# Performance work log

Hardware: AMD Instinct MI355X
Metric: run time of the kernel (lower is better)

## Reference

```python
import jax, jax.numpy as jnp
import numpy as np

B, L, E, H, RR, BIO, NT, V, R = 16, 128, 256, 256, 128, 64, 3, 30000, 25


def setup_inputs() -> dict:
    key = jax.random.key(0)
    ks = jax.random.split(key, 24)
    s = 0.05
    n = jax.random.normal
    inp = {
        'tokens': jax.random.randint(ks[0], (B, L), 0, V),
        'bio_gold': jax.random.randint(ks[1], (B, L), 0, NT),
        'selection_gold': jax.random.uniform(ks[2], (B, L, R, L), jnp.float32),
        'word_emb': n(ks[3], (V, E), jnp.float32) * s,
        'W_ih_f': n(ks[4], (4 * H, E), jnp.float32) * s,
        'W_hh_f': n(ks[5], (4 * H, H), jnp.float32) * s,
        'b_f': n(ks[6], (4 * H,), jnp.float32) * s,
        'W_ih_b': n(ks[7], (4 * H, E), jnp.float32) * s,
        'W_hh_b': n(ks[8], (4 * H, H), jnp.float32) * s,
        'b_b': n(ks[9], (4 * H,), jnp.float32) * s,
        'emi_W': n(ks[10], (NT, H), jnp.float32) * s,
        'emi_b': n(ks[11], (NT,), jnp.float32) * s,
        'bio_emb': n(ks[12], (NT + 1, BIO), jnp.float32) * s,
        'sel_u_W': n(ks[13], (RR, H + BIO), jnp.float32) * s,
        'sel_u_b': n(ks[14], (RR,), jnp.float32) * s,
        'sel_v_W': n(ks[15], (RR, H + BIO), jnp.float32) * s,
        'sel_v_b': n(ks[16], (RR,), jnp.float32) * s,
        'sel_uv_W': n(ks[17], (RR, 2 * RR), jnp.float32) * s,
        'sel_uv_b': n(ks[18], (RR,), jnp.float32) * s,
        'rel_emb': n(ks[19], (R, RR), jnp.float32) * s,
        'crf_start': n(ks[20], (NT,), jnp.float32) * s,
        'crf_end': n(ks[21], (NT,), jnp.float32) * s,
        'crf_trans': n(ks[22], (NT, NT), jnp.float32) * s,
    }
    return inp


def _lstm(x, W_ih, W_hh, b, reverse):
    # x: [B,L,E] -> hidden states [B,L,H]; PyTorch gate order i,f,g,o
    Bb = x.shape[0]
    Hh = W_hh.shape[1]
    xg = jnp.swapaxes(jnp.einsum('ble,ge->blg', x, W_ih) + b, 0, 1)  # [L,B,4H]

    def step(carry, xt):
        h, c = carry
        g = xt + h @ W_hh.T
        i, f, gg, o = jnp.split(g, 4, axis=-1)
        c = jax.nn.sigmoid(f) * c + jax.nn.sigmoid(i) * jnp.tanh(gg)
        h = jax.nn.sigmoid(o) * jnp.tanh(c)
        return (h, c), h

    init = (jnp.zeros((Bb, Hh), x.dtype), jnp.zeros((Bb, Hh), x.dtype))
    _, hs = jax.lax.scan(step, init, xg, reverse=reverse)
    return jnp.swapaxes(hs, 0, 1)


def reference(tokens, bio_gold, selection_gold, word_emb, W_ih_f, W_hh_f, b_f,
              W_ih_b, W_hh_b, b_b, emi_W, emi_b, bio_emb, sel_u_W, sel_u_b,
              sel_v_W, sel_v_b, sel_uv_W, sel_uv_b, rel_emb, crf_start,
              crf_end, crf_trans):
    mask = tokens != 0  # pad id 0
    maskf = mask.astype(jnp.float32)
    emb = word_emb[tokens]
    # BiLSTM, halves averaged as in (fwd + bwd) / 2
    o = (_lstm(emb, W_ih_f, W_hh_f, b_f, False)
         + _lstm(emb, W_ih_b, W_hh_b, b_b, True)) * 0.5
    emi = o @ emi_W.T + emi_b  # [B,L,NT]

    # ---- CRF negative log-likelihood (torchcrf, reduction='mean') ----
    bidx = jnp.arange(tokens.shape[0])
    e_sel = jnp.take_along_axis(emi, bio_gold[..., None], axis=2)[..., 0]  # [B,L]
    num = crf_start[bio_gold[:, 0]] + e_sel[:, 0]
    tr = crf_trans[bio_gold[:, :-1], bio_gold[:, 1:]]  # [B,L-1]
    num = num + ((tr + e_sel[:, 1:]) * maskf[:, 1:]).sum(1)
    seq_ends = jnp.maximum(mask.sum(1) - 1, 0)
    num = num + crf_end[bio_gold[bidx, seq_ends]]

    def crf_step(score, inp):
        emi_t, m_t = inp
        nxt = jax.nn.logsumexp(score[:, :, None] + crf_trans[None] + emi_t[:, None, :], axis=1)
        return jnp.where(m_t[:, None], nxt, score), None

    score0 = crf_start + emi[:, 0]
    score, _ = jax.lax.scan(crf_step, score0,
                            (jnp.swapaxes(emi[:, 1:], 0, 1), jnp.swapaxes(mask[:, 1:], 0, 1)))
    den = jax.nn.logsumexp(score + crf_end, axis=1)
    crf_loss = -(num - den).mean()

    # ---- pairwise biaffine selection head ----
    oc = jnp.concatenate([o, bio_emb[bio_gold]], axis=-1)  # [B,L,H+BIO]
    u = jax.nn.relu(oc @ sel_u_W.T + sel_u_b)  # [B,L,RR]
    v = jax.nn.relu(oc @ sel_v_W.T + sel_v_b)
    Rr = rel_emb.shape[1]
    W1, W2 = sel_uv_W[:, :Rr], sel_uv_W[:, Rr:]  # split cat([u,v]) linear
    a = u @ W1.T  # indexed by j (u was expanded along dim 1)
    c = v @ W2.T  # indexed by i
    uv = jax.nn.relu(a[:, None, :, :] + c[:, :, None, :] + sel_uv_b)  # [B,L,L,RR]
    logits = jnp.einsum('bijh,rh->birj', uv, rel_emb)  # [B,L,R,L]

    y = selection_gold
    bce = jnp.maximum(logits, 0) - logits * y + jnp.log1p(jnp.exp(-jnp.abs(logits)))
    selmask = maskf[:, :, None, None] * maskf[:, None, None, :]  # [B,L,1,L]
    sel_loss = (bce * selmask).sum() / maskf.sum()
    return crf_loss + sel_loss
```

## Files before the change

kernel.cpp:

```cpp
#include <hip/hip_runtime.h>
#include <cstdint>
#include <cstddef>


typedef __attribute__((ext_vector_type(8))) short short8;
typedef __attribute__((ext_vector_type(8))) int i32x8;
typedef __attribute__((ext_vector_type(4))) float f32x4;

__device__ __forceinline__ unsigned short f2bf(float f) {
  unsigned int u = __float_as_uint(f);
  u += 0x7fffu + ((u >> 16) & 1u);
  return (unsigned short)(u >> 16);
}
__device__ __forceinline__ float bf2f(unsigned short u) {
  return __uint_as_float(((unsigned int)u) << 16);
}

__device__ __forceinline__ void dev_pp8k128(const float* __restrict__ W,
                                            unsigned int* __restrict__ out, int idx) {
  int c = idx & 3;
  int lane = (idx >> 2) & 63;
  int f = idx >> 8;
  int nt = f >> 1, kt = f & 1;
  int n = nt * 16 + (lane & 15);
  int k0 = kt * 128 + (lane >> 4) * 32 + c * 8;
  const float* wp = &W[(size_t)n * 256 + k0];
  int lo = 0, hi = 0;
  lo = __builtin_amdgcn_cvt_pk_fp8_f32(wp[0], wp[1], lo, false);
  lo = __builtin_amdgcn_cvt_pk_fp8_f32(wp[2], wp[3], lo, true);
  hi = __builtin_amdgcn_cvt_pk_fp8_f32(wp[4], wp[5], hi, false);
  hi = __builtin_amdgcn_cvt_pk_fp8_f32(wp[6], wp[7], hi, true);
  size_t base = ((size_t)(f << 6) + lane) * 8 + (c << 1);
  out[base] = (unsigned)lo;
  out[base + 1] = (unsigned)hi;
}

__device__ __forceinline__ void dev_ppw(const float* __restrict__ W, int ldw, int nkt,
                                        uint4* __restrict__ out, int idx) {
  int lane = idx & 63;
  int f = idx >> 6;
  int kt = f % nkt;
  int nt = f / nkt;
  int row = nt * 16 + (lane & 15);
  int k0 = kt * 32 + ((lane >> 4) << 3);
  const float* wp = &W[(size_t)row * ldw + k0];
  union { unsigned short us[8]; uint4 v; } tmp;
#pragma unroll
  for (int j = 0; j < 8; ++j) tmp.us[j] = f2bf(wp[j]);
  out[idx] = tmp.v;
}

__global__ __launch_bounds__(256) void k_setup(
    const float* __restrict__ Whhf, unsigned int* __restrict__ wpk8f,
    const float* __restrict__ Whhb, unsigned int* __restrict__ wpk8b,
    const float* __restrict__ Wihf, uint4* __restrict__ wihfPk,
    const float* __restrict__ Wihb, uint4* __restrict__ wihbPk,
    const float* __restrict__ suW, uint4* __restrict__ suPk,
    const float* __restrict__ svW, uint4* __restrict__ svPk,
    const float* __restrict__ suvW, uint4* __restrict__ w1Pk, uint4* __restrict__ w2Pk,
    float* __restrict__ acc) {
  int bid = blockIdx.x;
  int t = threadIdx.x;
  if (bid < 128) {
    dev_pp8k128(Whhf, wpk8f, bid * 256 + t);
  } else if (bid < 256) {
    dev_pp8k128(Whhb, wpk8b, (bid - 128) * 256 + t);
  } else if (bid < 384) {
    dev_ppw(Wihf, 256, 8, wihfPk, (bid - 256) * 256 + t);
  } else if (bid < 512) {
    dev_ppw(Wihb, 256, 8, wihbPk, (bid - 384) * 256 + t);
  } else if (bid < 532) {
    dev_ppw(suW, 320, 10, suPk, (bid - 512) * 256 + t);
  } else if (bid < 552) {
    dev_ppw(svW, 320, 10, svPk, (bid - 532) * 256 + t);
  } else if (bid < 560) {
    dev_ppw(suvW, 256, 4, w1Pk, (bid - 552) * 256 + t);
  } else if (bid < 568) {
    dev_ppw(suvW + 128, 256, 4, w2Pk, (bid - 560) * 256 + t);
  } else {
    if (t < 16) acc[t] = 0.f;
  }
}

__global__ __launch_bounds__(256) void k_xg(
    const int* __restrict__ tok, const float* __restrict__ wemb,
    const uint4* __restrict__ WpkF, const float* __restrict__ biasF,
    unsigned short* __restrict__ CF,
    const uint4* __restrict__ WpkB, const float* __restrict__ biasB,
    unsigned short* __restrict__ CB) {
  const uint4* Wp = blockIdx.z ? WpkB : WpkF;
  const float* bi = blockIdx.z ? biasB : biasF;
  unsigned short* Co = blockIdx.z ? CB : CF;
  int bn = blockIdx.x, bm = blockIdx.y;
  int tid = threadIdx.x;
  int w = tid >> 6;
  int lane = tid & 63;
  int m = lane & 15;
  int q = lane >> 4;
  int arow = bm * 64 + w * 16 + m;
  const float* ew = wemb + (size_t)tok[arow] * 256 + (q << 3);
  f32x4 z = {0.f, 0.f, 0.f, 0.f};
  f32x4 ac[4] = {z, z, z, z};
  for (int kt = 0; kt < 8; ++kt) {
    float4 e0 = *reinterpret_cast<const float4*>(ew + (kt << 5));
    float4 e1 = *reinterpret_cast<const float4*>(ew + (kt << 5) + 4);
    union { unsigned short us[8]; short8 v; } af;
    af.us[0] = f2bf(e0.x); af.us[1] = f2bf(e0.y); af.us[2] = f2bf(e0.z); af.us[3] = f2bf(e0.w);
    af.us[4] = f2bf(e1.x); af.us[5] = f2bf(e1.y); af.us[6] = f2bf(e1.z); af.us[7] = f2bf(e1.w);
#pragma unroll
    for (int nt = 0; nt < 4; ++nt) {
      uint4 b4 = Wp[(size_t)(((bn << 2) + nt) * 8 + kt) * 64 + lane];
      ac[nt] = __builtin_amdgcn_mfma_f32_16x16x32_bf16(af.v, __builtin_bit_cast(short8, b4), ac[nt], 0, 0, 0);
    }
  }
#pragma unroll
  for (int nt = 0; nt < 4; ++nt) {
    int col = (bn << 6) + (nt << 4) + m;
    float bv = bi[col];
#pragma unroll
    for (int reg = 0; reg < 4; ++reg) {
      int row = (bm << 6) + (w << 4) + (q << 2) + reg;
      Co[(size_t)row * 1024 + col] = f2bf(ac[nt][reg] + bv);
    }
  }
}

__global__ __launch_bounds__(1024, 4) void k_lstm8(
    const unsigned short* __restrict__ xgf, const unsigned short* __restrict__ xgb,
    const unsigned int* __restrict__ wpkf, const unsigned int* __restrict__ wpkb,
    unsigned short* __restrict__ hsf, unsigned short* __restrict__ hsb) {
  int bid = blockIdx.x;
  int dir = bid >> 4;
  int b = bid & 15;
  const unsigned short* xg = (dir ? xgb : xgf) + (size_t)b * 128 * 1024;
  const unsigned int* wpk = dir ? wpkb : wpkf;
  unsigned short* hseq = (dir ? hsb : hsf) + (size_t)b * 128 * 256;

  __shared__ __align__(16) unsigned short xgl[8 * 1024];
  __shared__ __align__(16) unsigned short hfl[8 * 256];
  __shared__ __align__(16) unsigned char h8[2][16 * 272];

  int tid = threadIdx.x;
  int w = tid >> 6;
  int lane = tid & 63;
  int m = lane & 15;
  int q = lane >> 4;

  i32x8 wfr[4][2];
#pragma unroll
  for (int g = 0; g < 4; ++g)
#pragma unroll
    for (int kt = 0; kt < 2; ++kt) {
      int f = (((g << 4) + w) << 1) + kt;
      wfr[g][kt] = *reinterpret_cast<const i32x8*>(wpk + (((size_t)(f << 6) + lane) << 3));
    }
#pragma unroll
  for (int g = 0; g < 4; ++g)
#pragma unroll
    for (int kt = 0; kt < 2; ++kt)
      asm volatile("" : "+v"(wfr[g][kt]));

  for (int i = tid; i < 2 * 16 * 272 / 4; i += 1024) ((unsigned int*)&h8[0][0])[i] = 0;
  {
    int tb0 = dir ? 120 : 0;
    uint4 x0 = *reinterpret_cast<const uint4*>((const char*)xg + (size_t)tb0 * 2048 + tid * 16);
    reinterpret_cast<uint4*>(xgl)[tid] = x0;
  }
  __syncthreads();

  float cstate = 0.f;
  int j = (w << 4) + m;

  for (int c = 0; c < 16; ++c) {
    int tbase = dir ? (120 - 8 * c) : (8 * c);
    uint4 xnext = {0, 0, 0, 0};
    if (c < 15) {
      int tb2 = dir ? (tbase - 8) : (tbase + 8);
      xnext = *reinterpret_cast<const uint4*>((const char*)xg + (size_t)tb2 * 2048 + tid * 16);
    }
#pragma unroll
    for (int i = 0; i < 8; ++i) {
      int s = 8 * c + i;
      int t = dir ? (127 - s) : s;
      int slot = t & 7;
      const unsigned char* cur = h8[s & 1];
      unsigned char* nxt = h8[(s & 1) ^ 1];

      float x0 = 0.f, x1 = 0.f, x2 = 0.f, x3 = 0.f;
      if (q == 0) {
        const unsigned short* xb = xgl + slot * 1024 + j;
        x0 = bf2f(xb[0]);
        x1 = bf2f(xb[256]);
        x2 = bf2f(xb[512]);
        x3 = bf2f(xb[768]);
      }

      i32x8 afr[2];
#pragma unroll
      for (int kt = 0; kt < 2; ++kt) {
        union { uint4 u[2]; i32x8 v; } tmp;
        const unsigned char* hp = cur + m * 272 + kt * 128 + q * 32;
        tmp.u[0] = *reinterpret_cast<const uint4*>(hp);
        tmp.u[1] = *reinterpret_cast<const uint4*>(hp + 16);
        afr[kt] = tmp.v;
      }

      f32x4 zz = {0.f, 0.f, 0.f, 0.f};
      f32x4 acg[4] = {zz, zz, zz, zz};
#pragma unroll
      for (int kt = 0; kt < 2; ++kt)
#pragma unroll
        for (int g = 0; g < 4; ++g)
          acg[g] = __builtin_amdgcn_mfma_scale_f32_16x16x128_f8f6f4(
              afr[kt], wfr[g][kt], acg[g],
              0, 0, 0, 0x7f7f7f7f, 0, 0x7f7f7f7f);

      if (q == 0) {
        float gi = acg[0][0] + x0;
        float gf = acg[1][0] + x1;
        float gg = acg[2][0] + x2;
        float go = acg[3][0] + x3;
        gi = fminf(fmaxf(gi, -30.f), 30.f);
        gf = fminf(fmaxf(gf, -30.f), 30.f);
        gg = fminf(fmaxf(gg, -30.f), 30.f);
        go = fminf(fmaxf(go, -30.f), 30.f);
        float si = __fdividef(1.f, 1.f + __expf(-gi));
        float sf = __fdividef(1.f, 1.f + __expf(-gf));
        float so = __fdividef(1.f, 1.f + __expf(-go));
        float eg = __expf(-2.f * gg);
        float tg = __fdividef(1.f - eg, 1.f + eg);
        float cc2 = sf * cstate + si * tg;
        cstate = cc2;
        float cc = fminf(fmaxf(cc2, -30.f), 30.f);
        float ec = __expf(-2.f * cc);
        float th = __fdividef(1.f - ec, 1.f + ec);
        float h = so * th;
        hfl[slot * 256 + j] = f2bf(h);
        int pk = __builtin_amdgcn_cvt_pk_fp8_f32(h, h, 0, false);
        nxt[j] = (unsigned char)(pk & 0xff);
      }
      __syncthreads();
    }
    if (tid < 256) {
      int trow = tid >> 5;
      int j0 = (tid & 31) << 3;
      uint4 hv = reinterpret_cast<const uint4*>(hfl)[tid];
      *reinterpret_cast<uint4*>(hseq + (size_t)(tbase + trow) * 256 + j0) = hv;
    }
    if (c < 15) {
      reinterpret_cast<uint4*>(xgl)[tid] = xnext;
      __syncthreads();
    }
  }
}

__global__ __launch_bounds__(256) void k_mid2(
    const unsigned short* __restrict__ hf16, const unsigned short* __restrict__ hb16,
    const int* __restrict__ bio, const float* __restrict__ bioE,
    const float* __restrict__ emiW, const float* __restrict__ emib,
    const uint4* __restrict__ suPk, const float* __restrict__ sub,
    const uint4* __restrict__ svPk, const float* __restrict__ svb,
    const uint4* __restrict__ w1Pk, const uint4* __restrict__ w2Pk,
    unsigned short* __restrict__ a16, unsigned short* __restrict__ c16,
    float* __restrict__ emi) {
  __shared__ __align__(16) unsigned short oc[16][328];
  __shared__ __align__(16) unsigned short ub[16][136];
  __shared__ __align__(16) unsigned short vb[16][136];
  int r0 = blockIdx.x * 16;
  int tid = threadIdx.x;

#pragma unroll
  for (int it = 0; it < 8; ++it) {
    int i = it * 256 + tid;
    int row = i >> 7, h2 = (i & 127) << 1;
    unsigned int af = *reinterpret_cast<const unsigned int*>(hf16 + (size_t)(r0 + row) * 256 + h2);
    unsigned int ab = *reinterpret_cast<const unsigned int*>(hb16 + (size_t)(r0 + row) * 256 + h2);
    float lo = 0.5f * (bf2f((unsigned short)af) + bf2f((unsigned short)ab));
    float hi = 0.5f * (bf2f((unsigned short)(af >> 16)) + bf2f((unsigned short)(ab >> 16)));
    unsigned int pk = (unsigned int)f2bf(lo) | ((unsigned int)f2bf(hi) << 16);
    *reinterpret_cast<unsigned int*>(&oc[row][h2]) = pk;
  }
#pragma unroll
  for (int it = 0; it < 2; ++it) {
    int i = it * 256 + tid;
    int row = i >> 5, p = (i & 31) << 1;
    int bi = bio[r0 + row];
    float b0 = bioE[bi * 64 + p], b1 = bioE[bi * 64 + p + 1];
    unsigned int pk = (unsigned int)f2bf(b0) | ((unsigned int)f2bf(b1) << 16);
    *reinterpret_cast<unsigned int*>(&oc[row][256 + p]) = pk;
  }
  __syncthreads();

  if (tid < 192) {
    int did = tid >> 2, sub4 = tid & 3;
    int row = did / 3, g = did - row * 3;
    const float* ew = emiW + g * 256 + sub4 * 64;
    float av = 0.f;
#pragma unroll
    for (int k = 0; k < 64; ++k) av += bf2f(oc[row][sub4 * 64 + k]) * ew[k];
    av += __shfl_xor(av, 1);
    av += __shfl_xor(av, 2);
    if (sub4 == 0) emi[(size_t)(r0 + row) * 3 + g] = av + emib[g];
  }

  int w = tid >> 6, lane = tid & 63, m = lane & 15, q = lane >> 4;
  {
    f32x4 z = {0.f, 0.f, 0.f, 0.f};
    f32x4 au[2] = {z, z}, av2[2] = {z, z};
    for (int kt = 0; kt < 10; ++kt) {
      uint4 a4 = *reinterpret_cast<const uint4*>(&oc[m][(kt << 5) + (q << 3)]);
      short8 af = __builtin_bit_cast(short8, a4);
#pragma unroll
      for (int d = 0; d < 2; ++d) {
        int nt = (w << 1) + d;
        uint4 bu = suPk[(size_t)(nt * 10 + kt) * 64 + lane];
        uint4 bv = svPk[(size_t)(nt * 10 + kt) * 64 + lane];
        au[d] = __builtin_amdgcn_mfma_f32_16x16x32_bf16(af, __builtin_bit_cast(short8, bu), au[d], 0, 0, 0);
        av2[d] = __builtin_amdgcn_mfma_f32_16x16x32_bf16(af, __builtin_bit_cast(short8, bv), av2[d], 0, 0, 0);
      }
    }
#pragma unroll
    for (int d = 0; d < 2; ++d) {
      int col = ((w << 1) + d) * 16 + m;
      float bu = sub[col], bv = svb[col];
#pragma unroll
      for (int reg = 0; reg < 4; ++reg) {
        int row = (q << 2) + reg;
        ub[row][col] = f2bf(fmaxf(au[d][reg] + bu, 0.f));
        vb[row][col] = f2bf(fmaxf(av2[d][reg] + bv, 0.f));
      }
    }
  }
  __syncthreads();

  {
    f32x4 z = {0.f, 0.f, 0.f, 0.f};
    f32x4 aa[2] = {z, z}, cc[2] = {z, z};
    for (int kt = 0; kt < 4; ++kt) {
      uint4 ua = *reinterpret_cast<const uint4*>(&ub[m][(kt << 5) + (q << 3)]);
      uint4 va = *reinterpret_cast<const uint4*>(&vb[m][(kt << 5) + (q << 3)]);
      short8 uf = __builtin_bit_cast(short8, ua);
      short8 vf = __builtin_bit_cast(short8, va);
#pragma unroll
      for (int d = 0; d < 2; ++d) {
        int nt = (w << 1) + d;
        uint4 b1 = w1Pk[(size_t)((nt << 2) + kt) * 64 + lane];
        uint4 b2 = w2Pk[(size_t)((nt << 2) + kt) * 64 + lane];
        aa[d] = __builtin_amdgcn_mfma_f32_16x16x32_bf16(uf, __builtin_bit_cast(short8, b1), aa[d], 0, 0, 0);
        cc[d] = __builtin_amdgcn_mfma_f32_16x16x32_bf16(vf, __builtin_bit_cast(short8, b2), cc[d], 0, 0, 0);
      }
    }
#pragma unroll
    for (int d = 0; d < 2; ++d) {
      int col = ((w << 1) + d) * 16 + m;
#pragma unroll
      for (int reg = 0; reg < 4; ++reg) {
        int row = r0 + (q << 2) + reg;
        a16[(size_t)row * 128 + col] = f2bf(aa[d][reg]);
        c16[(size_t)row * 128 + col] = f2bf(cc[d][reg]);
      }
    }
  }
}

__global__ __launch_bounds__(256) void k_loss(
    const unsigned short* __restrict__ a16, const unsigned short* __restrict__ c16,
    const float* __restrict__ suvb, const float* __restrict__ rel,
    const float* __restrict__ y, const int* __restrict__ tok,
    const float* __restrict__ emi, const int* __restrict__ bio,
    const float* __restrict__ cstart, const float* __restrict__ cend,
    const float* __restrict__ ctrans,
    float* __restrict__ acc, float* __restrict__ out) {
  int blk = blockIdx.x;
  int tid = threadIdx.x;
  if (blk < 1024) {
    __shared__ unsigned short alds[128][136];
    __shared__ float cbs[2][128];
    __shared__ float red[4];
    int b = blk >> 6;
    int ip = blk & 63;
    int hh = tid & 127;
    int half = tid >> 7;
#pragma unroll
    for (int it = 0; it < 32; ++it) {
      int idx = it * 256 + tid;
      int jrow = idx >> 6;
      int h2 = (idx & 63) << 1;
      unsigned int av = *reinterpret_cast<const unsigned int*>(
          a16 + ((size_t)(b << 7) + jrow) * 128 + h2);
      alds[h2][jrow] = (unsigned short)av;
      alds[h2 + 1][jrow] = (unsigned short)(av >> 16);
    }
    {
      int i = (ip << 1) + half;
      cbs[half][hh] = bf2f(c16[(size_t)((b << 7) + i) * 128 + hh]) + suvb[hh];
    }
    __syncthreads();
    int i = (ip << 1) + half;
    int j = hh;
    float lg[25];
#pragma unroll
    for (int r = 0; r < 25; ++r) lg[r] = 0.f;
    for (int h = 0; h < 128; ++h) {
      float av = bf2f(alds[h][j]);
      float uv = fmaxf(av + cbs[half][h], 0.f);
#pragma unroll
      for (int r = 0; r < 25; ++r) lg[r] += uv * rel[r * 128 + h];
    }
    float mi = (tok[(b << 7) + i] != 0) ? 1.f : 0.f;
    float mj = (tok[(b << 7) + j] != 0) ? 1.f : 0.f;
    const float* yp = y + (size_t)((b << 7) + i) * 3200 + j;
    float bs = 0.f;
#pragma unroll
    for (int r = 0; r < 25; ++r) {
      float x = lg[r];
      float yv = yp[r * 128];
      bs += fmaxf(x, 0.f) - x * yv + __logf(1.f + __expf(-fabsf(x)));
    }
    bs *= mi * mj;
#pragma unroll
    for (int off = 32; off; off >>= 1) bs += __shfl_down(bs, off);
    if ((tid & 63) == 0) red[tid >> 6] = bs;
    __syncthreads();
    if (tid == 0) atomicAdd(&acc[0], red[0] + red[1] + red[2] + red[3]);
  } else {
    __shared__ float elds[128][4];
    __shared__ float msk[128];
    __shared__ int biol[128];
    __shared__ float r_t[2], r_m[2];
    int b = blk - 1024;
    int t = tid;
    if (t < 128) {
      biol[t] = bio[b * 128 + t];
      msk[t] = (tok[b * 128 + t] != 0) ? 1.f : 0.f;
#pragma unroll
      for (int g = 0; g < 3; ++g) elds[t][g] = emi[(b * 128 + t) * 3 + g];
    }
    __syncthreads();
    if (t < 128) {
      float m = msk[t];
      float term;
      if (t == 0)
        term = cstart[biol[0]] + elds[0][biol[0]];
      else
        term = (ctrans[biol[t - 1] * 3 + biol[t]] + elds[t][biol[t]]) * m;
      float ms = m;
#pragma unroll
      for (int off = 32; off; off >>= 1) {
        term += __shfl_down(term, off);
        ms += __shfl_down(ms, off);
      }
      if ((t & 63) == 0) { r_t[t >> 6] = term; r_m[t >> 6] = ms; }
    }
    __syncthreads();
    if (t == 0) {
      float num = r_t[0] + r_t[1];
      float msum = r_m[0] + r_m[1];
      int se = (int)msum - 1;
      if (se < 0) se = 0;
      num += cend[biol[se]];
      float tr[9];
#pragma unroll
      for (int i2 = 0; i2 < 9; ++i2) tr[i2] = ctrans[i2];
      float s0 = cstart[0] + elds[0][0];
      float s1 = cstart[1] + elds[0][1];
      float s2 = cstart[2] + elds[0][2];
      for (int tt = 1; tt < 128; ++tt) {
        float a0, a1, a2, mx, n0, n1, n2;
        a0 = s0 + tr[0]; a1 = s1 + tr[3]; a2 = s2 + tr[6];
        mx = fmaxf(a0, fmaxf(a1, a2));
        n0 = mx + __logf(__expf(a0 - mx) + __expf(a1 - mx) + __expf(a2 - mx)) + elds[tt][0];
        a0 = s0 + tr[1]; a1 = s1 + tr[4]; a2 = s2 + tr[7];
        mx = fmaxf(a0, fmaxf(a1, a2));
        n1 = mx + __logf(__expf(a0 - mx) + __expf(a1 - mx) + __expf(a2 - mx)) + elds[tt][1];
        a0 = s0 + tr[2]; a1 = s1 + tr[5]; a2 = s2 + tr[8];
        mx = fmaxf(a0, fmaxf(a1, a2));
        n2 = mx + __logf(__expf(a0 - mx) + __expf(a1 - mx) + __expf(a2 - mx)) + elds[tt][2];
        if (msk[tt] != 0.f) { s0 = n0; s1 = n1; s2 = n2; }
      }
      float a0 = s0 + cend[0], a1 = s1 + cend[1], a2 = s2 + cend[2];
      float mx = fmaxf(a0, fmaxf(a1, a2));
      float den = mx + __logf(__expf(a0 - mx) + __expf(a1 - mx) + __expf(a2 - mx));
      atomicAdd(&acc[1], num - den);
      atomicAdd(&acc[2], msum);
    }
  }
  if (tid == 0) {
    __threadfence();
    unsigned old = atomicAdd((unsigned int*)(acc + 5), 1u);
    if (old == 1039u) {
      __threadfence();
      float s0 = atomicAdd(&acc[0], 0.f);
      float s1 = atomicAdd(&acc[1], 0.f);
      float s2 = atomicAdd(&acc[2], 0.f);
      out[0] = -(s1 * (1.f / 16.f)) + s0 / s2;
    }
  }
}

extern "C" void kernel_launch(void* const* d_in, const int* in_sizes, int n_in,
                              void* d_out, int out_size, void* d_ws, size_t ws_size,
                              hipStream_t stream) {
  const int* tokens = (const int*)d_in[0];
  const int* bio = (const int*)d_in[1];
  const float* selg = (const float*)d_in[2];
  const float* wemb = (const float*)d_in[3];
  const float* Wihf = (const float*)d_in[4];
  const float* Whhf = (const float*)d_in[5];
  const float* bf = (const float*)d_in[6];
  const float* Wihb = (const float*)d_in[7];
  const float* Whhb = (const float*)d_in[8];
  const float* bb = (const float*)d_in[9];
  const float* emiW = (const float*)d_in[10];
  const float* emib = (const float*)d_in[11];
  const float* bioE = (const float*)d_in[12];
  const float* suW = (const float*)d_in[13];
  const float* sub = (const float*)d_in[14];
  const float* svW = (const float*)d_in[15];
  const float* svb = (const float*)d_in[16];
  const float* suvW = (const float*)d_in[17];
  const float* suvb = (const float*)d_in[18];
  const float* rel = (const float*)d_in[19];
  const float* cstart = (const float*)d_in[20];
  const float* cend = (const float*)d_in[21];
  const float* ctrans = (const float*)d_in[22];

  float* ws = (float*)d_ws;
  float* xgf16 = ws;
  float* xgb16 = xgf16 + 1048576;
  float* hf16 = xgb16 + 1048576;
  float* hb16 = hf16 + 262144;
  float* a16 = hb16 + 262144;
  float* c16 = a16 + 131072;
  float* emi = c16 + 131072;
  float* wpk8f = emi + 6144;
  float* wpk8b = wpk8f + 65536;
  float* wihfPk = wpk8b + 65536;
  float* wihbPk = wihfPk + 131072;
  float* suPk = wihbPk + 131072;
  float* svPk = suPk + 20480;
  float* w1Pk = svPk + 20480;
  float* w2Pk = w1Pk + 8192;
  float* acc = w2Pk + 8192;

  k_setup<<<569, 256, 0, stream>>>(
      Whhf, (unsigned int*)wpk8f, Whhb, (unsigned int*)wpk8b,
      Wihf, (uint4*)wihfPk, Wihb, (uint4*)wihbPk,
      suW, (uint4*)suPk, svW, (uint4*)svPk,
      suvW, (uint4*)w1Pk, (uint4*)w2Pk, acc);

  k_xg<<<dim3(16, 32, 2), 256, 0, stream>>>(
      tokens, wemb,
      (const uint4*)wihfPk, bf, (unsigned short*)xgf16,
      (const uint4*)wihbPk, bb, (unsigned short*)xgb16);

  k_lstm8<<<32, 1024, 0, stream>>>(
      (const unsigned short*)xgf16, (const unsigned short*)xgb16,
      (const unsigned int*)wpk8f, (const unsigned int*)wpk8b,
      (unsigned short*)hf16, (unsigned short*)hb16);

  k_mid2<<<128, 256, 0, stream>>>(
      (const unsigned short*)hf16, (const unsigned short*)hb16,
      bio, bioE, emiW, emib,
      (const uint4*)suPk, sub, (const uint4*)svPk, svb,
      (const uint4*)w1Pk, (const uint4*)w2Pk,
      (unsigned short*)a16, (unsigned short*)c16, emi);

  k_loss<<<1040, 256, 0, stream>>>((const unsigned short*)a16, (const unsigned short*)c16,
                                   suvb, rel, selg, tokens, emi, bio,
                                   cstart, cend, ctrans, acc, (float*)d_out);
}
```

Before: 394.4 us.

## Shrink LSTM recurrent buffer, fold xg into MFMA accumulator, lighten step barrier

The LSTM recurrence kernel now stores the fp8 hidden vector once per step (256 bytes) instead of replicating it across 16 padded rows, and every lane reads the same broadcast row as its MFMA A operand. The precomputed input gate term is preloaded into the MFMA accumulator, so no separate add is needed afterwards. The gate math drops its clamps, uses a cheaper tanh form, and runs on all lanes without a branch; only q==0 lanes write results. The per-step __syncthreads is replaced by an explicit LDS waitcnt plus s_barrier, aiming to cut the serial per-timestep latency. Removing the clamps relies on __expf overflow still giving correct saturation.

```diff
diff --git a/kernel.cpp b/kernel.cpp
--- a/kernel.cpp
+++ b/kernel.cpp
@@ -138,7 +138,7 @@
 
   __shared__ __align__(16) unsigned short xgl[8 * 1024];
   __shared__ __align__(16) unsigned short hfl[8 * 256];
-  __shared__ __align__(16) unsigned char h8[2][16 * 272];
+  __shared__ __align__(16) unsigned char h8[2][256];
 
   int tid = threadIdx.x;
   int w = tid >> 6;
@@ -160,11 +160,11 @@
     for (int kt = 0; kt < 2; ++kt)
       asm volatile("" : "+v"(wfr[g][kt]));
 
-  for (int i = tid; i < 2 * 16 * 272 / 4; i += 1024) ((unsigned int*)&h8[0][0])[i] = 0;
+  if (tid < 128) reinterpret_cast<unsigned int*>(&h8[0][0])[tid] = 0u;
   {
     int tb0 = dir ? 120 : 0;
-    uint4 x0 = *reinterpret_cast<const uint4*>((const char*)xg + (size_t)tb0 * 2048 + tid * 16);
-    reinterpret_cast<uint4*>(xgl)[tid] = x0;
+    uint4 x0v = *reinterpret_cast<const uint4*>((const char*)xg + (size_t)tb0 * 2048 + tid * 16);
+    reinterpret_cast<uint4*>(xgl)[tid] = x0v;
   }
   __syncthreads();
 
@@ -186,27 +186,27 @@
       const unsigned char* cur = h8[s & 1];
       unsigned char* nxt = h8[(s & 1) ^ 1];
 
-      float x0 = 0.f, x1 = 0.f, x2 = 0.f, x3 = 0.f;
-      if (q == 0) {
-        const unsigned short* xb = xgl + slot * 1024 + j;
-        x0 = bf2f(xb[0]);
-        x1 = bf2f(xb[256]);
-        x2 = bf2f(xb[512]);
-        x3 = bf2f(xb[768]);
-      }
+      const unsigned short* xb = xgl + slot * 1024 + j;
+      float x0 = bf2f(xb[0]);
+      float x1 = bf2f(xb[256]);
+      float x2 = bf2f(xb[512]);
+      float x3 = bf2f(xb[768]);
 
       i32x8 afr[2];
 #pragma unroll
       for (int kt = 0; kt < 2; ++kt) {
         union { uint4 u[2]; i32x8 v; } tmp;
-        const unsigned char* hp = cur + m * 272 + kt * 128 + q * 32;
+        const unsigned char* hp = cur + kt * 128 + q * 32;
         tmp.u[0] = *reinterpret_cast<const uint4*>(hp);
         tmp.u[1] = *reinterpret_cast<const uint4*>(hp + 16);
         afr[kt] = tmp.v;
       }
 
-      f32x4 zz = {0.f, 0.f, 0.f, 0.f};
-      f32x4 acg[4] = {zz, zz, zz, zz};
+      f32x4 acg[4];
+      acg[0] = (f32x4){x0, 0.f, 0.f, 0.f};
+      acg[1] = (f32x4){x1, 0.f, 0.f, 0.f};
+      acg[2] = (f32x4){x2, 0.f, 0.f, 0.f};
+      acg[3] = (f32x4){x3, 0.f, 0.f, 0.f};
 #pragma unroll
       for (int kt = 0; kt < 2; ++kt)
 #pragma unroll
@@ -215,31 +215,26 @@
               afr[kt], wfr[g][kt], acg[g],
               0, 0, 0, 0x7f7f7f7f, 0, 0x7f7f7f7f);
 
+      float gi = acg[0][0];
+      float gf = acg[1][0];
+      float gg = acg[2][0];
+      float go = acg[3][0];
+      float si = __fdividef(1.f, 1.f + __expf(-gi));
+      float sf = __fdividef(1.f, 1.f + __expf(-gf));
+      float so = __fdividef(1.f, 1.f + __expf(-go));
+      float tg = 1.f - __fdividef(2.f, __expf(2.f * gg) + 1.f);
+      float cc2 = sf * cstate + si * tg;
+      cstate = cc2;
+      float th = 1.f - __fdividef(2.f, __expf(2.f * cc2) + 1.f);
+      float h = so * th;
       if (q == 0) {
-        float gi = acg[0][0] + x0;
-        float gf = acg[1][0] + x1;
-        float gg = acg[2][0] + x2;
-        float go = acg[3][0] + x3;
-        gi = fminf(fmaxf(gi, -30.f), 30.f);
-        gf = fminf(fmaxf(gf, -30.f), 30.f);
-        gg = fminf(fmaxf(gg, -30.f), 30.f);
-        go = fminf(fmaxf(go, -30.f), 30.f);
-        float si = __fdividef(1.f, 1.f + __expf(-gi));
-        float sf = __fdividef(1.f, 1.f + __expf(-gf));
-        float so = __fdividef(1.f, 1.f + __expf(-go));
-        float eg = __expf(-2.f * gg);
-        float tg = __fdividef(1.f - eg, 1.f + eg);
-        float cc2 = sf * cstate + si * tg;
-        cstate = cc2;
-        float cc = fminf(fmaxf(cc2, -30.f), 30.f);
-        float ec = __expf(-2.f * cc);
-        float th = __fdividef(1.f - ec, 1.f + ec);
-        float h = so * th;
         hfl[slot * 256 + j] = f2bf(h);
         int pk = __builtin_amdgcn_cvt_pk_fp8_f32(h, h, 0, false);
         nxt[j] = (unsigned char)(pk & 0xff);
       }
-      __syncthreads();
+      asm volatile("s_waitcnt lgkmcnt(0)" ::: "memory");
+      __builtin_amdgcn_s_barrier();
+      asm volatile("" ::: "memory");
     }
     if (tid < 256) {
       int trow = tid >> 5;
```

New measurement: 380.5 us. 1.04x faster.
